# Kernel tuning notes

Hardware: AMD Instinct MI355X
Metric: run time of the kernel (lower is better)

The kernel has to match this reference:

```python
import jax, jax.numpy as jnp
import numpy as np

B, S, H, NL, DF, VF = 8, 2048, 8, 128, 64, 64
NF, HS = 1280, 33
FEAT = NF + HS
NLAYERS = 2
MAXLAP = 0.001


def setup_inputs() -> dict:
    key = jax.random.key(0)
    ks = jax.random.split(key, 11)
    u = lambda k, shape: jax.random.uniform(k, shape, jnp.float32, -0.01, 0.01)
    return {
        "latent_outputs": jax.random.normal(ks[0], (B, S, HS), jnp.float32),
        "masks": (jax.random.uniform(ks[1], (B, S, 1)) > 0.05).astype(jnp.float32),
        "x_embeds": jax.random.normal(ks[2], (B, S, NF), jnp.float32),
        "pos_embed": jax.random.normal(ks[3], (B, S, DF), jnp.float32),
        "collect_classes": u(ks[4], (1, VF * H, HS)),
        "query_linear": u(ks[5], (NLAYERS, 1, H, FEAT + 1, DF)),
        "key_linear": u(ks[6], (NLAYERS, 1, 1, FEAT + 1, DF)),
        "value_linear": u(ks[7], (NLAYERS, 1, H, FEAT + 1, VF)),
        "project_original": u(ks[8], (NLAYERS, 1, 1, FEAT + 1, VF)),
        "aggregation_params": u(ks[9], (NLAYERS, 1, H, 1, 1)),
        "collect_feats": u(ks[10], (NLAYERS - 1, VF * H, FEAT)),
    }


def _iterative_inv(mat, n_iter=6):
    I = jnp.eye(mat.shape[-1], dtype=mat.dtype)
    key = mat
    value = (1.0 / jnp.max(jnp.sum(key, axis=-2))) * jnp.swapaxes(key, -1, -2)
    for _ in range(n_iter):
        kv = key @ value
        value = 0.25 * value @ (13 * I - kv @ (15 * I - kv @ (7 * I - kv)))
    return value


def _compute_accum(values, masks, qw, kw, vw, agg):
    # values: [B,1,S,FEAT]; qw/vw: [1,H,FEAT+1,*], kw: [1,1,FEAT+1,DF]
    # NOTE: bias is the second-to-last row (as in the torch source, [..., -2:-1, :]).
    Eq = values @ qw[..., :-1, :] + qw[..., -2:-1, :]  # [B,H,S,DF]
    Ek = values @ kw[..., :-1, :] + kw[..., -2:-1, :]  # [B,1,S,DF]
    Ev = values @ vw[..., :-1, :] + vw[..., -2:-1, :]  # [B,H,S,VF]
    pos = jnp.arange(S)
    rel = jnp.abs(pos[None, None, None, :] - pos[None, None, :, None]).astype(values.dtype)
    sigmas = jnp.abs(agg) + MAXLAP          # [1,H,1,1]
    pos_mask = -sigmas * rel                # [1,H,S,S] Laplace position penalty
    scale = DF ** 0.25
    Eq = Eq / scale
    Ek = Ek / scale
    seg = S // NL
    q_land = Eq.reshape(Eq.shape[0], Eq.shape[1], NL, seg, DF).mean(-2)  # [B,H,NL,DF]
    k_land = Ek.reshape(Ek.shape[0], Ek.shape[1], NL, seg, DF).mean(-2)  # [B,1,NL,DF]
    pos_sel = pos_mask.reshape(1, H, NL, seg, S).mean(3)                 # [1,H,NL,S]
    kernel_1 = jax.nn.softmax(Eq @ jnp.swapaxes(k_land, -1, -2)
                              + jnp.swapaxes(pos_sel, -1, -2), axis=-1)  # [B,H,S,NL]
    pos_sel2 = pos_sel.reshape(1, H, NL, NL, seg).mean(-1)               # [1,H,NL,NL]
    kernel_2 = jax.nn.softmax(q_land @ jnp.swapaxes(k_land, -1, -2) + pos_sel2, axis=-1)
    scores = q_land @ jnp.swapaxes(Ek, -1, -2)                            # [B,H,NL,S]
    attn_mask = jnp.swapaxes(jnp.where(masks[:, None] == 0, -1e6, 0.0), -1, -2)  # [B,1,1,S]
    kernel_3 = jax.nn.softmax(scores + attn_mask + pos_sel, axis=-1)      # [B,H,NL,S]
    probs = kernel_1 @ _iterative_inv(kernel_2)                           # [B,H,S,NL]
    return probs @ (kernel_3 @ Ev)                                        # [B,H,S,VF]


def reference(latent_outputs, masks, x_embeds, pos_embed, collect_classes,
              query_linear, key_linear, value_linear, project_original,
              aggregation_params, collect_feats):
    cl = jax.nn.softmax(latent_outputs, axis=-1) * masks
    orig = jnp.concatenate([x_embeds, cl], axis=-1)[:, None]  # [B,1,S,FEAT]
    va = orig
    for layer in range(NLAYERS):
        va = _compute_accum(va, masks, query_linear[layer], key_linear[layer],
                            value_linear[layer], aggregation_params[layer])
        pw = project_original[layer, ..., :-1, :]
        pb = project_original[layer, ..., -2:-1, :]
        va = va + (orig @ pw + pb) / NLAYERS            # [B,H,S,VF]
        va = jnp.transpose(va, (0, 2, 1, 3)).reshape(B, S, H * VF)
        cw = collect_feats[layer] if layer < NLAYERS - 1 else collect_classes
        va = (va @ cw)[:, None]
    return va[:, 0] * masks  # [B,S,HS]
```

## Files before the change

kernel.cpp:

```cpp
#include <hip/hip_runtime.h>
#include <math.h>


namespace {

constexpr int B = 8, S = 2048, H = 8, NL = 128, DF = 64, VF = 64;
constexpr int NF = 1280, HS = 33, FEAT = 1313, FEATP = 1314;
constexpr int SEG = 16, HV = H * VF;
constexpr int KSF = 1344;
constexpr int NSPL = 4;
constexpr long ROWS = (long)B * S;
constexpr float INV_SCALE = 0.35355339059327373f;

typedef _Float16 f16;
typedef _Float16 f16x8 __attribute__((ext_vector_type(8)));
typedef _Float16 f16x4 __attribute__((ext_vector_type(4)));
typedef float f32x4 __attribute__((ext_vector_type(4)));

__global__ __launch_bounds__(256) void k_cl(
    const float* __restrict__ lat, const float* __restrict__ masks,
    float* __restrict__ cl)
{
  long row = (long)blockIdx.x * 4 + (threadIdx.x >> 6);
  int l = threadIdx.x & 63;
  float v = (l < HS) ? lat[row * HS + l] : -INFINITY;
  float m = v;
  #pragma unroll
  for (int o = 32; o; o >>= 1) m = fmaxf(m, __shfl_xor(m, o));
  float e = (l < HS) ? expf(v - m) : 0.f;
  float s = e;
  #pragma unroll
  for (int o = 32; o; o >>= 1) s += __shfl_xor(s, o);
  if (l < HS) cl[row * HS + l] = e / s * masks[row];
}

__global__ __launch_bounds__(256) void k_prep(
    const float* __restrict__ xemb, const float* __restrict__ cl,
    const float* __restrict__ qlin, const float* __restrict__ klin,
    const float* __restrict__ vlin, const float* __restrict__ plin,
    const float* __restrict__ cfeat, const float* __restrict__ ccls,
    f16* __restrict__ origA,
    f16* __restrict__ WQt, f16* __restrict__ WKt, f16* __restrict__ WVt,
    f16* __restrict__ WPt, f16* __restrict__ WCFt, f16* __restrict__ WCCt)
{
  long bid = blockIdx.x;
  int tid = threadIdx.x;
  if (bid < 10752) {
    long idx = bid * 256 + tid;
    long row = idx / 168;
    int c = (int)(idx - row * 168);
    int t = c >> 3, cs = c & 7;
    int k0 = t * 64 + cs * 8;
    f16x8 v;
    if (t < 20) {
      float4 a = *(const float4*)&xemb[row * NF + k0];
      float4 b = *(const float4*)&xemb[row * NF + k0 + 4];
      v[0] = (f16)a.x; v[1] = (f16)a.y; v[2] = (f16)a.z; v[3] = (f16)a.w;
      v[4] = (f16)b.x; v[5] = (f16)b.y; v[6] = (f16)b.z; v[7] = (f16)b.w;
    } else {
      #pragma unroll
      for (int i = 0; i < 8; ++i) {
        int k = k0 + i;
        float f = 0.f;
        if (k < NF) f = xemb[row * NF + k];
        else if (k < FEAT) f = cl[row * HS + (k - NF)];
        v[i] = (f16)f;
      }
    }
    int cd = cs ^ ((int)row & 7);
    *(f16x8*)&origA[row * KSF + t * 64 + cd * 8] = v;
  } else {
    constexpr long s1 = 172032, s2 = 193536, s3 = 365568, s4 = 387072,
                   s5 = 473088, s6 = 477184;
    long idx = (bid - 10752) * 256 + tid;
    if (idx >= s6) return;
    const float* src; f16* dst; int K, N, Npad, KS; long srcZ, rel;
    if (idx < s1)      { src = qlin;  dst = WQt;  K = FEAT; N = 64;  Npad = 64;  KS = KSF; srcZ = (long)FEATP * 64; rel = idx; }
    else if (idx < s2) { src = klin;  dst = WKt;  K = FEAT; N = 64;  Npad = 64;  KS = KSF; srcZ = (long)FEATP * 64; rel = idx - s1; }
    else if (idx < s3) { src = vlin;  dst = WVt;  K = FEAT; N = 64;  Npad = 64;  KS = KSF; srcZ = (long)FEATP * 64; rel = idx - s2; }
    else if (idx < s4) { src = plin;  dst = WPt;  K = FEAT; N = 64;  Npad = 64;  KS = KSF; srcZ = (long)FEATP * 64; rel = idx - s3; }
    else if (idx < s5) { src = cfeat; dst = WCFt; K = 512;  N = FEAT; Npad = KSF; KS = 512; srcZ = 0; rel = idx - s4; }
    else               { src = ccls;  dst = WCCt; K = 512;  N = HS;  Npad = 64;  KS = 512; srcZ = 0; rel = idx - s5; }
    long cpz = (long)Npad * (KS >> 3);
    long z = rel / cpz;
    long rem = rel - z * cpz;
    int n = (int)(rem / (KS >> 3));
    int c = (int)(rem - (long)n * (KS >> 3));
    int t = c >> 3, cs = c & 7;
    int cd = cs ^ (n & 7);
    int k0 = t * 64 + cd * 8;
    const float* sp = src + z * srcZ;
    f16x8 v;
    #pragma unroll
    for (int i = 0; i < 8; ++i) {
      int k = k0 + i;
      v[i] = (f16)((k < K && n < N) ? sp[(long)k * N + n] : 0.f);
    }
    *(f16x8*)&dst[rel * 8] = v;
  }
}

__global__ __launch_bounds__(256, 2) void k_mgemm(
    const f16* __restrict__ A, long aZOff, int aDiv,
    const f16* __restrict__ Wt, long wZOff, int wMod,
    int KT, int mode,
    float* __restrict__ C, long cZOff, int ldC,
    const float* __restrict__ biasBase, long biasZOff, float scale,
    f16* __restrict__ outA, int NR, const float* __restrict__ mask)
{
  const long KS = (long)KT * 64;
  int z = blockIdx.z;
  const f16* Ap = A + (long)(z / aDiv) * aZOff;
  const f16* Wp = Wt + (long)(z % wMod) * wZOff;
  long m0 = (long)blockIdx.x * 256;
  int n0 = blockIdx.y * 64;
  constexpr int BOFF = 256 * 64;
  __shared__ f16 lds[2][(256 + 64) * 64];
  int tid = threadIdx.x;
  int wv = tid >> 6, l = tid & 63;

  const f16* aW = Ap + (m0 + wv * 64 + (l >> 3)) * KS + (l & 7) * 8;
  const f16* bW = Wp + ((long)(n0 + wv * 16 + (l >> 3))) * KS + (l & 7) * 8;

  f32x4 acc[4][4];
  #pragma unroll
  for (int i = 0; i < 4; ++i)
    #pragma unroll
    for (int j = 0; j < 4; ++j) acc[i][j] = (f32x4){0.f, 0.f, 0.f, 0.f};

  auto stage = [&](int buf, int t) {
    f16* la = &lds[buf][(wv * 64) * 64];
    const f16* ga = aW + (long)t * 64;
    #pragma unroll
    for (int j = 0; j < 8; ++j)
      __builtin_amdgcn_global_load_lds(
          (const __attribute__((address_space(1))) void*)(ga + (long)j * 8 * KS),
          (__attribute__((address_space(3))) void*)(la + j * 8 * 64), 16, 0, 0);
    f16* lb = &lds[buf][BOFF + (wv * 16) * 64];
    const f16* gb = bW + (long)t * 64;
    #pragma unroll
    for (int j = 0; j < 2; ++j)
      __builtin_amdgcn_global_load_lds(
          (const __attribute__((address_space(1))) void*)(gb + (long)j * 8 * KS),
          (__attribute__((address_space(3))) void*)(lb + j * 8 * 64), 16, 0, 0);
  };

  stage(0, 0);
  int rA = (wv * 64 + (l & 15)) * 64;
  int rB = BOFF + (l & 15) * 64;
  int lc = l >> 4, lx = l & 7;
  for (int t = 0; t < KT; ++t) {
    int nb = t & 1;
    if (t + 1 < KT) {
      stage(nb ^ 1, t + 1);
      asm volatile("s_waitcnt vmcnt(10)" ::: "memory");
    } else {
      asm volatile("s_waitcnt vmcnt(0)" ::: "memory");
    }
    __syncthreads();
    const f16* base = &lds[nb][0];
    f16x8 af[4][2], bf[4][2];
    #pragma unroll
    for (int mi = 0; mi < 4; ++mi)
      #pragma unroll
      for (int kh = 0; kh < 2; ++kh)
        af[mi][kh] = *(const f16x8*)&base[rA + mi * 16 * 64 + (((kh * 4 + lc) ^ lx) << 3)];
    #pragma unroll
    for (int ni = 0; ni < 4; ++ni)
      #pragma unroll
      for (int kh = 0; kh < 2; ++kh)
        bf[ni][kh] = *(const f16x8*)&base[rB + ni * 16 * 64 + (((kh * 4 + lc) ^ lx) << 3)];
    #pragma unroll
    for (int mi = 0; mi < 4; ++mi)
      #pragma unroll
      for (int ni = 0; ni < 4; ++ni) {
        acc[mi][ni] = __builtin_amdgcn_mfma_f32_16x16x32_f16(af[mi][0], bf[ni][0], acc[mi][ni], 0, 0, 0);
        acc[mi][ni] = __builtin_amdgcn_mfma_f32_16x16x32_f16(af[mi][1], bf[ni][1], acc[mi][ni], 0, 0, 0);
      }
    __syncthreads();
  }

  int lr = (l >> 4) * 4;
  int lcn = l & 15;
  if (mode == 2) {
    #pragma unroll
    for (int mi = 0; mi < 4; ++mi) {
      #pragma unroll
      for (int r = 0; r < 4; ++r) {
        long row = m0 + wv * 64 + mi * 16 + lr + r;
        float mv = mask[row];
        #pragma unroll
        for (int ni = 0; ni < 4; ++ni) {
          int col = n0 + ni * 16 + lcn;
          if (col < NR) C[row * (long)ldC + col] = acc[mi][ni][r] * mv;
        }
      }
    }
  } else {
    f16* st = &lds[0][0];
    #pragma unroll
    for (int ni = 0; ni < 4; ++ni) {
      int coll = ni * 16 + lcn;
      int col = n0 + coll;
      bool ok = col < NR;
      #pragma unroll
      for (int mi = 0; mi < 4; ++mi) {
        int rowl = wv * 64 + mi * 16 + lr;
        #pragma unroll
        for (int r = 0; r < 4; ++r) {
          float v = ok ? acc[mi][ni][r] * scale : 0.f;
          st[(rowl + r) * 64 + coll] = (f16)v;
        }
      }
    }
    __syncthreads();
    int tt = n0 >> 6;
    for (int c = tid; c < 2048; c += 256) {
      int row = c >> 3, cd = c & 7;
      long grow = m0 + row;
      int r7 = (int)grow & 7;
      f16x8 v = *(const f16x8*)&st[row * 64 + cd * 8];
      *(f16x8*)&outA[grow * KSF + tt * 64 + ((cd ^ r7) << 3)] = v;
    }
  }
}

__global__ __launch_bounds__(256, 2) void k_qve(
    const f16* __restrict__ Aact, const f16* __restrict__ Aorig,
    const f16* __restrict__ WQl, const f16* __restrict__ WVl,
    const f16* __restrict__ wk, const f16* __restrict__ wp,
    const float* __restrict__ bqBase, const float* __restrict__ bvBase,
    const float* __restrict__ bk, const float* __restrict__ bp,
    f16* __restrict__ Eq16, f16* __restrict__ Ev16, f16* __restrict__ Ek16,
    float* __restrict__ projb,
    f16* __restrict__ qland16, f16* __restrict__ kland16)
{
  constexpr int KT = 21;
  __shared__ __align__(16) f16 shbuf[256 * 64];
  int bid = blockIdx.x;
  int tid = threadIdx.x;
  int wv = tid >> 6, l = tid & 63;
  int l15 = l & 15, lc = l >> 4, lx = l & 7;
  int lr = (l >> 4) * 4;
  int lcn = l & 15;

  if (bid < 1024) {
    constexpr int BOFF = 128 * 64;
    int z = bid >> 4;
    int h = z & 7;
    const f16* Ap = Aact + (long)(z >> 3) * S * KSF;
    const f16* wqp = WQl + (long)h * 64 * KSF;
    const f16* wvp = WVl + (long)h * 64 * KSF;
    const float* bq = bqBase + (long)h * FEATP * 64;
    const float* bv = bvBase + (long)h * FEATP * 64;
    long m0 = (long)(bid & 15) * 128;

    const f16* aW = Ap + (m0 + wv * 32 + (l >> 3)) * KSF + (l & 7) * 8;

    f32x4 acc[2][8];
    #pragma unroll
    for (int i = 0; i < 2; ++i)
      #pragma unroll
      for (int j = 0; j < 8; ++j) acc[i][j] = (f32x4){0.f, 0.f, 0.f, 0.f};

    auto stage = [&](int t) {
      f16* la = &shbuf[(wv * 32) * 64];
      const f16* ga = aW + (long)t * 64;
      #pragma unroll
      for (int j = 0; j < 4; ++j)
        __builtin_amdgcn_global_load_lds(
            (const __attribute__((address_space(1))) void*)(ga + (long)j * 8 * KSF),
            (__attribute__((address_space(3))) void*)(la + j * 512), 16, 0, 0);
      f16* lb = &shbuf[BOFF + (wv * 32) * 64];
      #pragma unroll
      for (int j = 0; j < 4; ++j) {
        int brow = wv * 32 + j * 8 + (l >> 3);
        const f16* src = (brow < 64 ? wqp + (long)brow * KSF
                                    : wvp + (long)(brow - 64) * KSF)
                         + (l & 7) * 8 + (long)t * 64;
        __builtin_amdgcn_global_load_lds(
            (const __attribute__((address_space(1))) void*)src,
            (__attribute__((address_space(3))) void*)(lb + j * 512), 16, 0, 0);
      }
    };

    for (int t = 0; t < KT; ++t) {
      stage(t);
      asm volatile("s_waitcnt vmcnt(0)" ::: "memory");
      __syncthreads();
      const f16* base = &shbuf[0];
      f16x8 af[2][2], bf[8][2];
      #pragma unroll
      for (int mi = 0; mi < 2; ++mi)
        #pragma unroll
        for (int kh = 0; kh < 2; ++kh)
          af[mi][kh] = *(const f16x8*)&base[(wv * 32 + mi * 16 + l15) * 64 + (((kh * 4 + lc) ^ lx) << 3)];
      #pragma unroll
      for (int ni = 0; ni < 8; ++ni) {
        int n = ni * 16 + l15;
        #pragma unroll
        for (int kh = 0; kh < 2; ++kh)
          bf[ni][kh] = *(const f16x8*)&base[BOFF + n * 64 + (((kh * 4 + lc) ^ (n & 7)) << 3)];
      }
      #pragma unroll
      for (int mi = 0; mi < 2; ++mi)
        #pragma unroll
        for (int ni = 0; ni < 8; ++ni) {
          acc[mi][ni] = __builtin_amdgcn_mfma_f32_16x16x32_f16(af[mi][0], bf[ni][0], acc[mi][ni], 0, 0, 0);
          acc[mi][ni] = __builtin_amdgcn_mfma_f32_16x16x32_f16(af[mi][1], bf[ni][1], acc[mi][ni], 0, 0, 0);
        }
      __syncthreads();
    }

    f16* st = &shbuf[0];
    #pragma unroll
    for (int ni = 0; ni < 8; ++ni) {
      int col = ni * 16 + l15;
      float bvv = (col < 64) ? bq[col] : bv[col - 64];
      float scl = (col < 64) ? INV_SCALE : 1.f;
      #pragma unroll
      for (int mi = 0; mi < 2; ++mi) {
        int rowl = wv * 32 + mi * 16 + lr;
        #pragma unroll
        for (int r = 0; r < 4; ++r)
          st[(rowl + r) * 128 + col] = (f16)((acc[mi][ni][r] + bvv) * scl);
      }
    }
    __syncthreads();
    f16* oq = Eq16 + (long)z * S * 64;
    f16* ov = Ev16 + (long)z * S * 64;
    for (int c = tid; c < 1024; c += 256) {
      int rw = c >> 3, cc = c & 7;
      *(f16x8*)&oq[(m0 + rw) * 64 + cc * 8] = *(const f16x8*)&st[rw * 128 + cc * 8];
      *(f16x8*)&ov[(m0 + rw) * 64 + cc * 8] = *(const f16x8*)&st[rw * 128 + 64 + cc * 8];
    }
    for (int c = tid; c < 512; c += 256) {
      int lm = c >> 6, d = c & 63;
      float s = 0.f;
      #pragma unroll
      for (int i = 0; i < SEG; ++i) s += (float)st[(lm * SEG + i) * 128 + d];
      float v = s * (1.f / SEG);
      long li = (long)z * NL + (m0 >> 4) + lm;
      qland16[li * 64 + d] = (f16)v;
    }
  } else {
    constexpr int BOFF = 128 * 64;
    int rel = bid - 1024;
    int zz2 = rel >> 4;
    int prob = zz2 >> 3, b = zz2 & 7;
    const f16* Ap = (prob ? Aorig : Aact) + (long)b * S * KSF;
    const f16* Wp = prob ? wp : wk;
    long m0 = (long)(rel & 15) * 128;

    const f16* aW = Ap + (m0 + wv * 32 + (l >> 3)) * KSF + (l & 7) * 8;
    const f16* bW = Wp + ((long)(wv * 16 + (l >> 3))) * KSF + (l & 7) * 8;

    f32x4 acc[2][4];
    #pragma unroll
    for (int i = 0; i < 2; ++i)
      #pragma unroll
      for (int j = 0; j < 4; ++j) acc[i][j] = (f32x4){0.f, 0.f, 0.f, 0.f};

    auto stage = [&](int t) {
      f16* la = &shbuf[(wv * 32) * 64];
      const f16* ga = aW + (long)t * 64;
      #pragma unroll
      for (int j = 0; j < 4; ++j)
        __builtin_amdgcn_global_load_lds(
            (const __attribute__((address_space(1))) void*)(ga + (long)j * 8 * KSF),
            (__attribute__((address_space(3))) void*)(la + j * 512), 16, 0, 0);
      f16* lb = &shbuf[BOFF + (wv * 16) * 64];
      const f16* gb = bW + (long)t * 64;
      #pragma unroll
      for (int j = 0; j < 2; ++j)
        __builtin_amdgcn_global_load_lds(
            (const __attribute__((address_space(1))) void*)(gb + (long)j * 8 * KSF),
            (__attribute__((address_space(3))) void*)(lb + j * 512), 16, 0, 0);
    };

    for (int t = 0; t < KT; ++t) {
      stage(t);
      asm volatile("s_waitcnt vmcnt(0)" ::: "memory");
      __syncthreads();
      const f16* base = &shbuf[0];
      f16x8 af[2][2], bf[4][2];
      #pragma unroll
      for (int mi = 0; mi < 2; ++mi)
        #pragma unroll
        for (int kh = 0; kh < 2; ++kh)
          af[mi][kh] = *(const f16x8*)&base[(wv * 32 + mi * 16 + l15) * 64 + (((kh * 4 + lc) ^ lx) << 3)];
      #pragma unroll
      for (int ni = 0; ni < 4; ++ni)
        #pragma unroll
        for (int kh = 0; kh < 2; ++kh)
          bf[ni][kh] = *(const f16x8*)&base[BOFF + (ni * 16 + l15) * 64 + (((kh * 4 + lc) ^ lx) << 3)];
      #pragma unroll
      for (int mi = 0; mi < 2; ++mi)
        #pragma unroll
        for (int ni = 0; ni < 4; ++ni) {
          acc[mi][ni] = __builtin_amdgcn_mfma_f32_16x16x32_f16(af[mi][0], bf[ni][0], acc[mi][ni], 0, 0, 0);
          acc[mi][ni] = __builtin_amdgcn_mfma_f32_16x16x32_f16(af[mi][1], bf[ni][1], acc[mi][ni], 0, 0, 0);
        }
      __syncthreads();
    }

    if (prob == 0) {
      f16* st = &shbuf[0];
      #pragma unroll
      for (int ni = 0; ni < 4; ++ni) {
        int col = ni * 16 + lcn;
        float bv = bk[col];
        #pragma unroll
        for (int mi = 0; mi < 2; ++mi) {
          int rowl = wv * 32 + mi * 16 + lr;
          #pragma unroll
          for (int r = 0; r < 4; ++r)
            st[(rowl + r) * 64 + col] = (f16)((acc[mi][ni][r] + bv) * INV_SCALE);
        }
      }
      __syncthreads();
      f16* o16 = Ek16 + (long)b * S * 64;
      for (int c = tid; c < 1024; c += 256) {
        int row = c >> 3, cc = c & 7;
        f16x8 v = *(const f16x8*)&st[row * 64 + cc * 8];
        *(f16x8*)&o16[(m0 + row) * 64 + cc * 8] = v;
      }
      for (int c = tid; c < 512; c += 256) {
        int lm = c >> 6, d = c & 63;
        float s = 0.f;
        #pragma unroll
        for (int i = 0; i < SEG; ++i) s += (float)st[(lm * SEG + i) * 64 + d];
        float v = s * (1.f / SEG);
        long li = (long)b * NL + (m0 >> 4) + lm;
        kland16[li * 64 + d] = (f16)v;
      }
    } else {
      float* Cp = projb + (long)b * S * 64;
      #pragma unroll
      for (int ni = 0; ni < 4; ++ni) {
        int col = ni * 16 + lcn;
        float bv = bp[col];
        #pragma unroll
        for (int mi = 0; mi < 2; ++mi) {
          long row = m0 + wv * 32 + mi * 16 + lr;
          #pragma unroll
          for (int r = 0; r < 4; ++r)
            Cp[(row + r) * 64 + col] = (acc[mi][ni][r] + bv) * 0.5f;
        }
      }
    }
  }
}

__global__ __launch_bounds__(256, 2) void k_land(
    const f16* __restrict__ qland16, const f16* __restrict__ kland16,
    const f16* __restrict__ Ek16, const f16* __restrict__ Ev16,
    const float* __restrict__ aggL, const float* __restrict__ masks,
    float* __restrict__ partU, float* __restrict__ partML,
    f16* __restrict__ k2h, float* __restrict__ colmax)
{
  __shared__ __align__(16) unsigned char smem[57856];
  int bid = blockIdx.x;
  int tid = threadIdx.x;
  int w = tid >> 6, l = tid & 63;
  int l15 = l & 15, lg4 = l >> 4, l7 = l & 7;

  if (bid < 512) {
    f16* Qs = (f16*)smem;
    f16* Ks = (f16*)(smem + 8192);
    f16* Vt = (f16*)(smem + 24576);
    f16* Pb = (f16*)(smem + 40960);
    float* Ms = (float*)(smem + 57344);
    int chunk = bid & (NSPL - 1);
    int z2 = bid >> 2;
    int z = z2 >> 1, half = z2 & 1;
    int b = z >> 3, h = z & 7;
    int q0 = half * 64;
    float sigma = fabsf(aggL[h]) + 0.001f;
    float cpos = -sigma * (1.f / 16.f);

    for (int c = tid; c < 64 * 8; c += 256) {
      int q = c >> 3, kc = c & 7;
      f16x8 v = *(const f16x8*)&qland16[((long)z * NL + q0 + q) * 64 + kc * 8];
      *(f16x8*)&Qs[q * 64 + ((kc ^ (q & 7)) << 3)] = v;
    }

    f16* Pw = &Pb[w * 16 * 128];
    f32x4 Oa[4];
    #pragma unroll
    for (int i = 0; i < 4; ++i) Oa[i] = (f32x4){0.f, 0.f, 0.f, 0.f};
    float mrun[4] = {-INFINITY, -INFINITY, -INFINITY, -INFINITY};
    float lrun[4] = {0.f, 0.f, 0.f, 0.f};

    int t0beg = chunk * (S / 128 / NSPL), t0end = t0beg + S / 128 / NSPL;
    for (int t0 = t0beg; t0 < t0end; ++t0) {
      __syncthreads();
      for (int c = tid; c < 1024; c += 256) {
        int k = c >> 3, kc = c & 7;
        f16x8 v = *(const f16x8*)&Ek16[((long)b * S + t0 * 128 + k) * 64 + kc * 8];
        *(f16x8*)&Ks[k * 64 + ((kc ^ (k & 7)) << 3)] = v;
      }
      for (int c = tid; c < 1024; c += 256) {
        int k = c & 127, dc = c >> 7;
        f16x8 v = *(const f16x8*)&Ev16[((long)z * S + t0 * 128 + k) * 64 + dc * 8];
        int kc = k >> 3, ki = k & 7;
        #pragma unroll
        for (int j = 0; j < 8; ++j) {
          int d = dc * 8 + j;
          Vt[d * 128 + ((kc ^ (d & 7)) << 3) + ki] = v[j];
        }
      }
      if (tid < 128)
        Ms[tid] = (masks[(long)b * S + t0 * 128 + tid] == 0.f) ? -1e6f : 0.f;
      __syncthreads();

      f16x8 af[2];
      #pragma unroll
      for (int kh = 0; kh < 2; ++kh)
        af[kh] = *(const f16x8*)&Qs[(w * 16 + l15) * 64 + (((kh * 4 + lg4) ^ l7) << 3)];
      f32x4 sc[8];
      #pragma unroll
      for (int ct = 0; ct < 8; ++ct) {
        int n = ct * 16 + l15;
        f16x8 b0 = *(const f16x8*)&Ks[n * 64 + (((lg4) ^ (n & 7)) << 3)];
        f16x8 b1 = *(const f16x8*)&Ks[n * 64 + (((4 + lg4) ^ (n & 7)) << 3)];
        f32x4 zz = (f32x4){0.f, 0.f, 0.f, 0.f};
        zz = __builtin_amdgcn_mfma_f32_16x16x32_f16(af[0], b0, zz, 0, 0, 0);
        sc[ct] = __builtin_amdgcn_mfma_f32_16x16x32_f16(af[1], b1, zz, 0, 0, 0);
      }
      float tmax[4] = {-INFINITY, -INFINITY, -INFINITY, -INFINITY};
      #pragma unroll
      for (int ct = 0; ct < 8; ++ct) {
        float mk = Ms[ct * 16 + l15];
        int key = t0 * 128 + ct * 16 + l15;
        #pragma unroll
        for (int r = 0; r < 4; ++r) {
          int qg = q0 + w * 16 + lg4 * 4 + r;
          float a = (float)(key - 16 * qg);
          float ac = fminf(fmaxf(a, 0.f), 15.f);
          float dd = fabsf(a - ac);
          float sum = ac * ac - 15.f * ac + 120.f + 16.f * dd;
          float s = sc[ct][r] + cpos * sum + mk;
          sc[ct][r] = s;
          tmax[r] = fmaxf(tmax[r], s);
        }
      }
      #pragma unroll
      for (int r = 0; r < 4; ++r) {
        #pragma unroll
        for (int o = 1; o < 16; o <<= 1)
          tmax[r] = fmaxf(tmax[r], __shfl_xor(tmax[r], o));
      }
      float fr[4], lsum[4];
      #pragma unroll
      for (int r = 0; r < 4; ++r) {
        float mnew = fmaxf(mrun[r], tmax[r]);
        fr[r] = expf(mrun[r] - mnew);
        mrun[r] = mnew;
        lsum[r] = 0.f;
      }
      #pragma unroll
      for (int ct = 0; ct < 8; ++ct) {
        #pragma unroll
        for (int r = 0; r < 4; ++r) {
          float p = expf(sc[ct][r] - mrun[r]);
          sc[ct][r] = p;
          lsum[r] += p;
        }
      }
      #pragma unroll
      for (int r = 0; r < 4; ++r) {
        #pragma unroll
        for (int o = 1; o < 16; o <<= 1)
          lsum[r] += __shfl_xor(lsum[r], o);
        lrun[r] = lrun[r] * fr[r] + lsum[r];
      }
      f32x4 fv = (f32x4){fr[0], fr[1], fr[2], fr[3]};
      #pragma unroll
      for (int dt = 0; dt < 4; ++dt) Oa[dt] *= fv;
      #pragma unroll
      for (int ct = 0; ct < 8; ++ct) {
        int kc = ct * 2 + (l15 >> 3);
        int ki = l15 & 7;
        #pragma unroll
        for (int r = 0; r < 4; ++r) {
          int row = lg4 * 4 + r;
          Pw[row * 128 + ((kc ^ (row & 7)) << 3) + ki] = (f16)sc[ct][r];
        }
      }
      #pragma unroll
      for (int ks = 0; ks < 4; ++ks) {
        f16x8 pa = *(const f16x8*)&Pw[l15 * 128 + (((ks * 4 + lg4) ^ l7) << 3)];
        #pragma unroll
        for (int dt = 0; dt < 4; ++dt) {
          int n = dt * 16 + l15;
          f16x8 bv = *(const f16x8*)&Vt[n * 128 + (((ks * 4 + lg4) ^ (n & 7)) << 3)];
          Oa[dt] = __builtin_amdgcn_mfma_f32_16x16x32_f16(pa, bv, Oa[dt], 0, 0, 0);
        }
      }
    }
    #pragma unroll
    for (int r = 0; r < 4; ++r) {
      long qg = q0 + w * 16 + lg4 * 4 + r;
      long base = ((long)z * NL + qg) * NSPL + chunk;
      #pragma unroll
      for (int dt = 0; dt < 4; ++dt)
        partU[base * 64 + dt * 16 + l15] = Oa[dt][r];
      if (l15 == 0) {
        partML[base * 2] = mrun[r];
        partML[base * 2 + 1] = lrun[r];
      }
    }
  } else {
    f16* Qs2 = (f16*)smem;
    f16* Ks2 = (f16*)(smem + 16384);
    float* colpart = (float*)(smem + 32768);
    int z = bid - 512;
    int b2 = z >> 3, h2 = z & 7;
    float sigma = fabsf(aggL[h2]) + 0.001f;
    for (int c = tid; c < 1024; c += 256) {
      int q = c >> 3, kc = c & 7;
      f16x8 v = *(const f16x8*)&qland16[((long)z * NL + q) * 64 + kc * 8];
      *(f16x8*)&Qs2[q * 64 + ((kc ^ (q & 7)) << 3)] = v;
      f16x8 u = *(const f16x8*)&kland16[((long)b2 * NL + q) * 64 + kc * 8];
      *(f16x8*)&Ks2[q * 64 + ((kc ^ (q & 7)) << 3)] = u;
    }
    __syncthreads();
    f32x4 acc[2][8];
    #pragma unroll
    for (int i = 0; i < 2; ++i)
      #pragma unroll
      for (int j = 0; j < 8; ++j) acc[i][j] = (f32x4){0.f, 0.f, 0.f, 0.f};
    f16x8 af[2][2];
    #pragma unroll
    for (int mi = 0; mi < 2; ++mi)
      #pragma unroll
      for (int kh = 0; kh < 2; ++kh)
        af[mi][kh] = *(const f16x8*)&Qs2[(w * 32 + mi * 16 + l15) * 64 + (((kh * 4 + lg4) ^ l7) << 3)];
    #pragma unroll
    for (int ni = 0; ni < 8; ++ni) {
      int n = ni * 16 + l15;
      f16x8 b0 = *(const f16x8*)&Ks2[n * 64 + ((lg4 ^ (n & 7)) << 3)];
      f16x8 b1 = *(const f16x8*)&Ks2[n * 64 + (((4 + lg4) ^ (n & 7)) << 3)];
      #pragma unroll
      for (int mi = 0; mi < 2; ++mi) {
        acc[mi][ni] = __builtin_amdgcn_mfma_f32_16x16x32_f16(af[mi][0], b0, acc[mi][ni], 0, 0, 0);
        acc[mi][ni] = __builtin_amdgcn_mfma_f32_16x16x32_f16(af[mi][1], b1, acc[mi][ni], 0, 0, 0);
      }
    }
    float colp[8];
    #pragma unroll
    for (int ni = 0; ni < 8; ++ni) colp[ni] = 0.f;
    f16* o2 = k2h + (long)z * NL * NL;
    #pragma unroll
    for (int mi = 0; mi < 2; ++mi) {
      float tmax[4] = {-INFINITY, -INFINITY, -INFINITY, -INFINITY};
      #pragma unroll
      for (int ni = 0; ni < 8; ++ni) {
        int m = ni * 16 + l15;
        #pragma unroll
        for (int r = 0; r < 4; ++r) {
          int row = w * 32 + mi * 16 + lg4 * 4 + r;
          float dd = fabsf((float)(row - m));
          float s = acc[mi][ni][r] - sigma * ((row == m) ? 5.3125f : 16.f * dd);
          acc[mi][ni][r] = s;
          tmax[r] = fmaxf(tmax[r], s);
        }
      }
      #pragma unroll
      for (int r = 0; r < 4; ++r) {
        #pragma unroll
        for (int o = 1; o < 16; o <<= 1)
          tmax[r] = fmaxf(tmax[r], __shfl_xor(tmax[r], o));
      }
      float lsum2[4] = {0.f, 0.f, 0.f, 0.f};
      #pragma unroll
      for (int ni = 0; ni < 8; ++ni)
        #pragma unroll
        for (int r = 0; r < 4; ++r) {
          float e = expf(acc[mi][ni][r] - tmax[r]);
          acc[mi][ni][r] = e;
          lsum2[r] += e;
        }
      #pragma unroll
      for (int r = 0; r < 4; ++r) {
        #pragma unroll
        for (int o = 1; o < 16; o <<= 1)
          lsum2[r] += __shfl_xor(lsum2[r], o);
        lsum2[r] = 1.f / lsum2[r];
      }
      #pragma unroll
      for (int ni = 0; ni < 8; ++ni) {
        int m = ni * 16 + l15;
        #pragma unroll
        for (int r = 0; r < 4; ++r) {
          float p = acc[mi][ni][r] * lsum2[r];
          o2[(long)(w * 32 + mi * 16 + lg4 * 4 + r) * NL + m] = (f16)p;
          colp[ni] += p;
        }
      }
    }
    #pragma unroll
    for (int ni = 0; ni < 8; ++ni) {
      colp[ni] += __shfl_xor(colp[ni], 16);
      colp[ni] += __shfl_xor(colp[ni], 32);
    }
    if (lg4 == 0) {
      #pragma unroll
      for (int ni = 0; ni < 8; ++ni)
        colpart[w * 128 + ni * 16 + l15] = colp[ni];
    }
    __syncthreads();
    if (tid < 128) {
      float cs = colpart[tid] + colpart[128 + tid] + colpart[256 + tid] + colpart[384 + tid];
      float wm = cs;
      #pragma unroll
      for (int o = 32; o; o >>= 1) wm = fmaxf(wm, __shfl_xor(wm, o));
      if ((tid & 63) == 0) colpart[512 + (tid >> 6)] = wm;
    }
    __syncthreads();
    if (tid == 0) colmax[z] = fmaxf(colpart[512], colpart[513]);
  }
}

__global__ __launch_bounds__(512) void k_inverse(
    const f16* __restrict__ k2h, const float* __restrict__ colmax,
    const float* __restrict__ partU, const float* __restrict__ partML,
    float* __restrict__ m2)
{
  __shared__ __align__(16) f16 bufA[128 * 128];
  __shared__ __align__(16) f16 bufB[128 * 128];
  __shared__ __align__(16) f16 Vt[128 * 128];
  __shared__ __align__(16) f16 Pt[128 * 128];
  int z = blockIdx.x;
  int tid = threadIdx.x;
  int w = tid >> 6, l = tid & 63;
  int l15 = l & 15, lg4 = l >> 4;
  int wr = (w >> 1) * 32, wc = (w & 1) * 64;

  float cv = colmax[l];
  #pragma unroll
  for (int o = 32; o; o >>= 1) cv = fmaxf(cv, __shfl_xor(cv, o));
  float recip = 1.f / cv;

  const f16* key = k2h + (long)z * NL * NL;
  auto swz = [](int r, int c) { return r * 128 + ((((c >> 3) ^ (r & 15))) << 3) + (c & 7); };

  for (int idx = tid; idx < 128 * 16; idx += 512) {
    int r = idx >> 4, c8 = (idx & 15) << 3;
    f16x8 kk = *(const f16x8*)&key[r * 128 + c8];
    f16x8 sv;
    #pragma unroll
    for (int j = 0; j < 8; ++j) sv[j] = (f16)(recip * (float)kk[j]);
    *(f16x8*)&Vt[swz(r, c8)] = sv;
    #pragma unroll
    for (int j = 0; j < 8; ++j) bufA[swz(c8 + j, r)] = sv[j];
  }
  __syncthreads();

  f16* Vc = bufA;
  f16* Sc = bufB;

  f32x4 acc[2][4];
  auto MMc = [&](bool fromGlobal, const f16* Aimg, const f16* Bimg) {
    #pragma unroll
    for (int mi = 0; mi < 2; ++mi)
      #pragma unroll
      for (int ni = 0; ni < 4; ++ni) acc[mi][ni] = (f32x4){0.f, 0.f, 0.f, 0.f};
    #pragma unroll
    for (int ks = 0; ks < 4; ++ks) {
      int k0 = ks * 32 + lg4 * 8;
      f16x8 bf[4];
      #pragma unroll
      for (int ni = 0; ni < 4; ++ni)
        bf[ni] = *(const f16x8*)&Bimg[swz(wc + ni * 16 + l15, k0)];
      f16x8 af[2];
      if (fromGlobal) {
        af[0] = *(const f16x8*)&key[(wr + l15) * 128 + k0];
        af[1] = *(const f16x8*)&key[(wr + 16 + l15) * 128 + k0];
      } else {
        af[0] = *(const f16x8*)&Aimg[swz(wr + l15, k0)];
        af[1] = *(const f16x8*)&Aimg[swz(wr + 16 + l15, k0)];
      }
      #pragma unroll
      for (int mi = 0; mi < 2; ++mi)
        #pragma unroll
        for (int ni = 0; ni < 4; ++ni)
          acc[mi][ni] = __builtin_amdgcn_mfma_f32_16x16x32_f16(af[mi], bf[ni], acc[mi][ni], 0, 0, 0);
    }
  };
  auto store = [&](f16* Nout, f16* Tout, float aT, float bT) {
    #pragma unroll
    for (int mi = 0; mi < 2; ++mi) {
      int row0 = wr + mi * 16 + lg4 * 4;
      #pragma unroll
      for (int ni = 0; ni < 4; ++ni) {
        int col = wc + ni * 16 + l15;
        f16x4 tv;
        #pragma unroll
        for (int r = 0; r < 4; ++r) {
          float v = acc[mi][ni][r];
          if (Nout) Nout[swz(row0 + r, col)] = (f16)v;
          tv[r] = (f16)(aT * v + ((row0 + r == col) ? bT : 0.f));
        }
        *(f16x4*)&Tout[col * 128 + ((((row0 >> 3) ^ (col & 15))) << 3) + (row0 & 7)] = tv;
      }
    }
  };

  for (int it = 0; it < 6; ++it) {
    MMc(true, nullptr, Vt);  store(Sc, Pt, -1.f, 7.f);       __syncthreads();
    MMc(false, Sc, Pt);      store(nullptr, Vt, -1.f, 15.f); __syncthreads();
    MMc(false, Sc, Vt);      store(nullptr, Pt, -0.25f, 3.25f); __syncthreads();
    MMc(false, Vc, Pt);      store(Sc, Vt, 1.f, 0.f);        __syncthreads();
    f16* tsw = Vc; Vc = Sc; Sc = tsw;
  }

  for (int idx = tid; idx < 128 * 16; idx += 512) {
    int q = idx >> 4, c4 = (idx & 15) << 2;
    long base = ((long)z * NL + q) * NSPL;
    float m[NSPL], lv[NSPL];
    #pragma unroll
    for (int c = 0; c < NSPL; ++c) {
      m[c] = partML[(base + c) * 2];
      lv[c] = partML[(base + c) * 2 + 1];
    }
    float M = fmaxf(fmaxf(m[0], m[1]), fmaxf(m[2], m[3]));
    float L = 0.f, scf[NSPL];
    #pragma unroll
    for (int c = 0; c < NSPL; ++c) {
      scf[c] = expf(m[c] - M);
      L += lv[c] * scf[c];
    }
    float4 o = make_float4(0.f, 0.f, 0.f, 0.f);
    #pragma unroll
    for (int c = 0; c < NSPL; ++c) {
      float4 u = *(const float4*)&partU[(base + c) * 64 + c4];
      o.x += scf[c] * u.x; o.y += scf[c] * u.y;
      o.z += scf[c] * u.z; o.w += scf[c] * u.w;
    }
    float invL = 1.f / L;
    Pt[swz(c4 + 0, q)] = (f16)(o.x * invL);
    Pt[swz(c4 + 1, q)] = (f16)(o.y * invL);
    Pt[swz(c4 + 2, q)] = (f16)(o.z * invL);
    Pt[swz(c4 + 3, q)] = (f16)(o.w * invL);
  }
  __syncthreads();
  f32x4 accF[4];
  #pragma unroll
  for (int ni = 0; ni < 4; ++ni) accF[ni] = (f32x4){0.f, 0.f, 0.f, 0.f};
  #pragma unroll
  for (int ks = 0; ks < 4; ++ks) {
    int k0 = ks * 32 + lg4 * 8;
    f16x8 af = *(const f16x8*)&Vc[swz(w * 16 + l15, k0)];
    #pragma unroll
    for (int ni = 0; ni < 4; ++ni) {
      f16x8 bf = *(const f16x8*)&Pt[swz(ni * 16 + l15, k0)];
      accF[ni] = __builtin_amdgcn_mfma_f32_16x16x32_f16(af, bf, accF[ni], 0, 0, 0);
    }
  }
  float* mp = m2 + (long)z * NL * VF;
  #pragma unroll
  for (int ni = 0; ni < 4; ++ni)
    #pragma unroll
    for (int r = 0; r < 4; ++r)
      mp[(long)(w * 16 + lg4 * 4 + r) * VF + ni * 16 + l15] = accF[ni][r];
}

__global__ __launch_bounds__(256, 2) void k_k1attn(
    const f16* __restrict__ Eq16, const f16* __restrict__ kland16,
    const float* __restrict__ aggL, const float* __restrict__ m2,
    const float* __restrict__ proj, f16* __restrict__ merged)
{
  __shared__ __align__(16) f16 Kl[128 * 64];
  __shared__ __align__(16) f16 M2t[64 * 128];
  __shared__ __align__(16) f16 Pb[4 * 16 * 128];
  int zz = blockIdx.x;
  int z = zz >> 5, st = zz & 31;
  int b = z >> 3, h = z & 7;
  int s0 = st * 64;
  int tid = threadIdx.x;
  int w = tid >> 6, l = tid & 63;
  int l15 = l & 15, lg4 = l >> 4, l7 = l & 7;
  float sigma = fabsf(aggL[h]) + 0.001f;
  float cpos = -sigma * (1.f / 16.f);

  for (int c = tid; c < 128 * 8; c += 256) {
    int k = c >> 3, kc = c & 7;
    f16x8 v = *(const f16x8*)&kland16[((long)b * NL + k) * 64 + kc * 8];
    *(f16x8*)&Kl[k * 64 + ((kc ^ (k & 7)) << 3)] = v;
  }
  const float* mp = m2 + (long)z * NL * VF;
  for (int c = tid; c < 128 * 16; c += 256) {
    int k = c >> 4, c4 = (c & 15) << 2;
    float4 v4 = *(const float4*)&mp[k * 64 + c4];
    int kc = k >> 3, ki = k & 7;
    M2t[(c4 + 0) * 128 + ((kc ^ ((c4 + 0) & 7)) << 3) + ki] = (f16)v4.x;
    M2t[(c4 + 1) * 128 + ((kc ^ ((c4 + 1) & 7)) << 3) + ki] = (f16)v4.y;
    M2t[(c4 + 2) * 128 + ((kc ^ ((c4 + 2) & 7)) << 3) + ki] = (f16)v4.z;
    M2t[(c4 + 3) * 128 + ((kc ^ ((c4 + 3) & 7)) << 3) + ki] = (f16)v4.w;
  }
  __syncthreads();

  long qrow = (long)z * S + s0 + w * 16 + l15;
  f16x8 af[2];
  #pragma unroll
  for (int kh = 0; kh < 2; ++kh)
    af[kh] = *(const f16x8*)&Eq16[qrow * 64 + kh * 32 + lg4 * 8];

  f32x4 sc[8];
  #pragma unroll
  for (int ct = 0; ct < 8; ++ct) {
    int n = ct * 16 + l15;
    f16x8 b0 = *(const f16x8*)&Kl[n * 64 + ((lg4 ^ (n & 7)) << 3)];
    f16x8 b1 = *(const f16x8*)&Kl[n * 64 + (((4 + lg4) ^ (n & 7)) << 3)];
    f32x4 zz4 = (f32x4){0.f, 0.f, 0.f, 0.f};
    zz4 = __builtin_amdgcn_mfma_f32_16x16x32_f16(af[0], b0, zz4, 0, 0, 0);
    sc[ct] = __builtin_amdgcn_mfma_f32_16x16x32_f16(af[1], b1, zz4, 0, 0, 0);
  }
  float tmax[4] = {-INFINITY, -INFINITY, -INFINITY, -INFINITY};
  #pragma unroll
  for (int ct = 0; ct < 8; ++ct) {
    int lm = ct * 16 + l15;
    #pragma unroll
    for (int r = 0; r < 4; ++r) {
      int spos = s0 + w * 16 + lg4 * 4 + r;
      float a = (float)(spos - 16 * lm);
      float ac = fminf(fmaxf(a, 0.f), 15.f);
      float dd = fabsf(a - ac);
      float sum = ac * ac - 15.f * ac + 120.f + 16.f * dd;
      float s = sc[ct][r] + cpos * sum;
      sc[ct][r] = s;
      tmax[r] = fmaxf(tmax[r], s);
    }
  }
  #pragma unroll
  for (int r = 0; r < 4; ++r) {
    #pragma unroll
    for (int o = 1; o < 16; o <<= 1)
      tmax[r] = fmaxf(tmax[r], __shfl_xor(tmax[r], o));
  }
  float lsum[4] = {0.f, 0.f, 0.f, 0.f};
  #pragma unroll
  for (int ct = 0; ct < 8; ++ct) {
    #pragma unroll
    for (int r = 0; r < 4; ++r) {
      float p = expf(sc[ct][r] - tmax[r]);
      sc[ct][r] = p;
      lsum[r] += p;
    }
  }
  #pragma unroll
  for (int r = 0; r < 4; ++r) {
    #pragma unroll
    for (int o = 1; o < 16; o <<= 1)
      lsum[r] += __shfl_xor(lsum[r], o);
    lsum[r] = 1.f / lsum[r];
  }
  f16* Pw = &Pb[w * 16 * 128];
  #pragma unroll
  for (int ct = 0; ct < 8; ++ct) {
    int kc = ct * 2 + (l15 >> 3);
    int ki = l15 & 7;
    #pragma unroll
    for (int r = 0; r < 4; ++r) {
      int row = lg4 * 4 + r;
      Pw[row * 128 + ((kc ^ (row & 7)) << 3) + ki] = (f16)(sc[ct][r] * lsum[r]);
    }
  }
  f32x4 Oa[4];
  #pragma unroll
  for (int i = 0; i < 4; ++i) Oa[i] = (f32x4){0.f, 0.f, 0.f, 0.f};
  #pragma unroll
  for (int ks = 0; ks < 4; ++ks) {
    f16x8 pa = *(const f16x8*)&Pw[l15 * 128 + (((ks * 4 + lg4) ^ l7) << 3)];
    #pragma unroll
    for (int dt = 0; dt < 4; ++dt) {
      int n = dt * 16 + l15;
      f16x8 bv = *(const f16x8*)&M2t[n * 128 + (((ks * 4 + lg4) ^ (n & 7)) << 3)];
      Oa[dt] = __builtin_amdgcn_mfma_f32_16x16x32_f16(pa, bv, Oa[dt], 0, 0, 0);
    }
  }
  #pragma unroll
  for (int r = 0; r < 4; ++r) {
    long srow = (long)b * S + s0 + w * 16 + lg4 * 4 + r;
    int r7 = (int)(srow & 7);
    #pragma unroll
    for (int dt = 0; dt < 4; ++dt) {
      int col = dt * 16 + l15;
      float v = Oa[dt][r] + proj[srow * VF + col];
      merged[srow * (long)HV + h * 64 + (((col >> 3) ^ r7) << 3) + (col & 7)] = (f16)v;
    }
  }
}

}

extern "C" void kernel_launch(void* const* d_in, const int* in_sizes, int n_in,
                              void* d_out, int out_size, void* d_ws, size_t ws_size,
                              hipStream_t stream)
{
  const float* lat   = (const float*)d_in[0];
  const float* masks = (const float*)d_in[1];
  const float* xemb  = (const float*)d_in[2];
  const float* ccls  = (const float*)d_in[4];
  const float* qlin  = (const float*)d_in[5];
  const float* klin  = (const float*)d_in[6];
  const float* vlin  = (const float*)d_in[7];
  const float* plin  = (const float*)d_in[8];
  const float* agg   = (const float*)d_in[9];
  const float* cfeat = (const float*)d_in[10];
  float* out = (float*)d_out;
  float* ws = (float*)d_ws;

  long off = 0;
  auto allocF = [&](long n) { float* p = ws + off; off += (n + 3) & ~3L; return p; };
  auto allocH = [&](long n) { f16* p = (f16*)(ws + off); off += ((n + 1) / 2 + 3) & ~3L; return p; };

  f16* origA = allocH(ROWS * KSF);
  f16* vbufA = allocH(ROWS * KSF);
  f16* merged = allocH(ROWS * (long)HV);
  f16* WQt = allocH(16L * 64 * KSF);
  f16* WKt = allocH(2L * 64 * KSF);
  f16* WVt = allocH(16L * 64 * KSF);
  f16* WPt = allocH(2L * 64 * KSF);
  f16* WCFt = allocH((long)KSF * 512);
  f16* WCCt = allocH(64L * 512);
  f16* Ek16 = allocH((long)B * S * 64);
  f16* Ev16 = allocH((long)B * H * S * 64);
  f16* Eq16 = allocH((long)B * H * S * 64);
  f16* qland16 = allocH((long)B * H * NL * DF);
  f16* kland16 = allocH((long)B * NL * DF);
  f16* k2h = allocH((long)B * H * NL * NL);
  float* cl     = allocF(ROWS * HS);
  float* projb  = allocF((long)B * S * VF);
  float* m2b    = allocF((long)B * H * NL * VF);
  float* colmax = allocF(64);
  float* partU  = allocF((long)B * H * NL * NSPL * 64);
  float* partML = allocF((long)B * H * NL * NSPL * 2);

  k_cl<<<(int)(ROWS / 4), 256, 0, stream>>>(lat, masks, cl);
  k_prep<<<10752 + 1864, 256, 0, stream>>>(xemb, cl, qlin, klin, vlin, plin,
      cfeat, ccls, origA, WQt, WKt, WVt, WPt, WCFt, WCCt);

  const f16* Aact = origA;
  for (int layer = 0; layer < 2; ++layer) {
    const f16* wq = WQt + (long)layer * 8 * 64 * KSF;
    const f16* wk = WKt + (long)layer * 64 * KSF;
    const f16* wvv = WVt + (long)layer * 8 * 64 * KSF;
    const f16* wp = WPt + (long)layer * 64 * KSF;
    const float* bq = qlin + (long)layer * 8 * FEATP * 64 + (long)(FEATP - 2) * 64;
    const float* bk = klin + (long)layer * FEATP * 64 + (long)(FEATP - 2) * 64;
    const float* bv = vlin + (long)layer * 8 * FEATP * 64 + (long)(FEATP - 2) * 64;
    const float* bp = plin + (long)layer * FEATP * 64 + (long)(FEATP - 2) * 64;
    const float* ag = agg + layer * H;

    k_qve<<<1280, 256, 0, stream>>>(Aact, origA, wq, wvv, wk, wp,
        bq, bv, bk, bp, Eq16, Ev16, Ek16, projb, qland16, kland16);

    k_land<<<576, 256, 0, stream>>>(qland16, kland16, Ek16, Ev16, ag, masks,
        partU, partML, k2h, colmax);
    k_inverse<<<B * H, 512, 0, stream>>>(k2h, colmax, partU, partML, m2b);
    k_k1attn<<<B * H * (S / 64), 256, 0, stream>>>(Eq16, kland16, ag, m2b, projb, merged);

    if (layer == 0) {
      dim3 gC(64, 21, 1);
      k_mgemm<<<gC, 256, 0, stream>>>(merged, 0, 1, WCFt, 0, 1, 8, 1,
          nullptr, 0, 0, nullptr, 0, 1.0f, vbufA, FEAT, nullptr);
      Aact = vbufA;
    } else {
      dim3 gO(64, 1, 1);
      k_mgemm<<<gO, 256, 0, stream>>>(merged, 0, 1, WCCt, 0, 1, 8, 2,
          out, 0, HS, nullptr, 0, 1.0f, nullptr, HS, masks);
    }
  }
  (void)in_sizes; (void)n_in; (void)out_size; (void)ws_size;
}
```

Before: 433.7 us.

## Process all 128 landmark queries per block and split keys eight ways

Each landmark-attention block now handles both 64-query halves against the same staged K/V tile, so K and V are loaded into shared memory once for all 128 queries instead of twice. To keep the block count at 512, the key dimension is split into 8 chunks instead of 4, and the merge step now reduces over 8 partials. The cost is more per-thread register state (two sets of accumulators), larger shared memory per block, and more partial results to combine.

```diff
diff --git a/kernel.cpp b/kernel.cpp
--- a/kernel.cpp
+++ b/kernel.cpp
@@ -8,7 +8,7 @@
 constexpr int NF = 1280, HS = 33, FEAT = 1313, FEATP = 1314;
 constexpr int SEG = 16, HV = H * VF;
 constexpr int KSF = 1344;
-constexpr int NSPL = 4;
+constexpr int NSPL = 8;
 constexpr long ROWS = (long)B * S;
 constexpr float INV_SCALE = 0.35355339059327373f;
 
@@ -459,7 +459,7 @@
     float* __restrict__ partU, float* __restrict__ partML,
     f16* __restrict__ k2h, float* __restrict__ colmax)
 {
-  __shared__ __align__(16) unsigned char smem[57856];
+  __shared__ __align__(16) unsigned char smem[66048];
   int bid = blockIdx.x;
   int tid = threadIdx.x;
   int w = tid >> 6, l = tid & 63;
@@ -467,30 +467,33 @@
 
   if (bid < 512) {
     f16* Qs = (f16*)smem;
-    f16* Ks = (f16*)(smem + 8192);
-    f16* Vt = (f16*)(smem + 24576);
-    f16* Pb = (f16*)(smem + 40960);
-    float* Ms = (float*)(smem + 57344);
+    f16* Ks = (f16*)(smem + 16384);
+    f16* Vt = (f16*)(smem + 32768);
+    f16* Pb = (f16*)(smem + 49152);
+    float* Ms = (float*)(smem + 65536);
     int chunk = bid & (NSPL - 1);
-    int z2 = bid >> 2;
-    int z = z2 >> 1, half = z2 & 1;
+    int z = bid >> 3;
     int b = z >> 3, h = z & 7;
-    int q0 = half * 64;
     float sigma = fabsf(aggL[h]) + 0.001f;
     float cpos = -sigma * (1.f / 16.f);
 
-    for (int c = tid; c < 64 * 8; c += 256) {
+    for (int c = tid; c < 128 * 8; c += 256) {
       int q = c >> 3, kc = c & 7;
-      f16x8 v = *(const f16x8*)&qland16[((long)z * NL + q0 + q) * 64 + kc * 8];
+      f16x8 v = *(const f16x8*)&qland16[((long)z * NL + q) * 64 + kc * 8];
       *(f16x8*)&Qs[q * 64 + ((kc ^ (q & 7)) << 3)] = v;
     }
 
     f16* Pw = &Pb[w * 16 * 128];
-    f32x4 Oa[4];
-    #pragma unroll
-    for (int i = 0; i < 4; ++i) Oa[i] = (f32x4){0.f, 0.f, 0.f, 0.f};
-    float mrun[4] = {-INFINITY, -INFINITY, -INFINITY, -INFINITY};
-    float lrun[4] = {0.f, 0.f, 0.f, 0.f};
+    f32x4 Oa[2][4];
+    float mrun[2][4], lrun[2][4];
+    #pragma unroll
+    for (int hf = 0; hf < 2; ++hf)
+      #pragma unroll
+      for (int i = 0; i < 4; ++i) {
+        Oa[hf][i] = (f32x4){0.f, 0.f, 0.f, 0.f};
+        mrun[hf][i] = -INFINITY;
+        lrun[hf][i] = 0.f;
+      }
 
     int t0beg = chunk * (S / 128 / NSPL), t0end = t0beg + S / 128 / NSPL;
     for (int t0 = t0beg; t0 < t0end; ++t0) {
@@ -514,101 +517,108 @@
         Ms[tid] = (masks[(long)b * S + t0 * 128 + tid] == 0.f) ? -1e6f : 0.f;
       __syncthreads();
 
-      f16x8 af[2];
-      #pragma unroll
-      for (int kh = 0; kh < 2; ++kh)
-        af[kh] = *(const f16x8*)&Qs[(w * 16 + l15) * 64 + (((kh * 4 + lg4) ^ l7) << 3)];
-      f32x4 sc[8];
-      #pragma unroll
-      for (int ct = 0; ct < 8; ++ct) {
-        int n = ct * 16 + l15;
-        f16x8 b0 = *(const f16x8*)&Ks[n * 64 + (((lg4) ^ (n & 7)) << 3)];
-        f16x8 b1 = *(const f16x8*)&Ks[n * 64 + (((4 + lg4) ^ (n & 7)) << 3)];
-        f32x4 zz = (f32x4){0.f, 0.f, 0.f, 0.f};
-        zz = __builtin_amdgcn_mfma_f32_16x16x32_f16(af[0], b0, zz, 0, 0, 0);
-        sc[ct] = __builtin_amdgcn_mfma_f32_16x16x32_f16(af[1], b1, zz, 0, 0, 0);
-      }
-      float tmax[4] = {-INFINITY, -INFINITY, -INFINITY, -INFINITY};
-      #pragma unroll
-      for (int ct = 0; ct < 8; ++ct) {
-        float mk = Ms[ct * 16 + l15];
-        int key = t0 * 128 + ct * 16 + l15;
+      #pragma unroll
+      for (int hf = 0; hf < 2; ++hf) {
+        int q0 = hf * 64;
+        f16x8 af[2];
+        #pragma unroll
+        for (int kh = 0; kh < 2; ++kh)
+          af[kh] = *(const f16x8*)&Qs[(q0 + w * 16 + l15) * 64 + (((kh * 4 + lg4) ^ l7) << 3)];
+        f32x4 sc[8];
+        #pragma unroll
+        for (int ct = 0; ct < 8; ++ct) {
+          int n = ct * 16 + l15;
+          f16x8 b0 = *(const f16x8*)&Ks[n * 64 + (((lg4) ^ (n & 7)) << 3)];
+          f16x8 b1 = *(const f16x8*)&Ks[n * 64 + (((4 + lg4) ^ (n & 7)) << 3)];
+          f32x4 zz = (f32x4){0.f, 0.f, 0.f, 0.f};
+          zz = __builtin_amdgcn_mfma_f32_16x16x32_f16(af[0], b0, zz, 0, 0, 0);
+          sc[ct] = __builtin_amdgcn_mfma_f32_16x16x32_f16(af[1], b1, zz, 0, 0, 0);
+        }
+        float tmax[4] = {-INFINITY, -INFINITY, -INFINITY, -INFINITY};
+        #pragma unroll
+        for (int ct = 0; ct < 8; ++ct) {
+          float mk = Ms[ct * 16 + l15];
+          int key = t0 * 128 + ct * 16 + l15;
+          #pragma unroll
+          for (int r = 0; r < 4; ++r) {
+            int qg = q0 + w * 16 + lg4 * 4 + r;
+            float a = (float)(key - 16 * qg);
+            float ac = fminf(fmaxf(a, 0.f), 15.f);
+            float dd = fabsf(a - ac);
+            float sum = ac * ac - 15.f * ac + 120.f + 16.f * dd;
+            float s = sc[ct][r] + cpos * sum + mk;
+            sc[ct][r] = s;
+            tmax[r] = fmaxf(tmax[r], s);
+          }
+        }
         #pragma unroll
         for (int r = 0; r < 4; ++r) {
-          int qg = q0 + w * 16 + lg4 * 4 + r;
-          float a = (float)(key - 16 * qg);
-          float ac = fminf(fmaxf(a, 0.f), 15.f);
-          float dd = fabsf(a - ac);
-          float sum = ac * ac - 15.f * ac + 120.f + 16.f * dd;
-          float s = sc[ct][r] + cpos * sum + mk;
-          sc[ct][r] = s;
-          tmax[r] = fmaxf(tmax[r], s);
-        }
-      }
+          #pragma unroll
+          for (int o = 1; o < 16; o <<= 1)
+            tmax[r] = fmaxf(tmax[r], __shfl_xor(tmax[r], o));
+        }
+        float fr[4], lsum[4];
+        #pragma unroll
+        for (int r = 0; r < 4; ++r) {
+          float mnew = fmaxf(mrun[hf][r], tmax[r]);
+          fr[r] = expf(mrun[hf][r] - mnew);
+          mrun[hf][r] = mnew;
+          lsum[r] = 0.f;
+        }
+        #pragma unroll
+        for (int ct = 0; ct < 8; ++ct) {
+          #pragma unroll
+          for (int r = 0; r < 4; ++r) {
+            float p = expf(sc[ct][r] - mrun[hf][r]);
+            sc[ct][r] = p;
+            lsum[r] += p;
+          }
+        }
+        #pragma unroll
+        for (int r = 0; r < 4; ++r) {
+          #pragma unroll
+          for (int o = 1; o < 16; o <<= 1)
+            lsum[r] += __shfl_xor(lsum[r], o);
+          lrun[hf][r] = lrun[hf][r] * fr[r] + lsum[r];
+        }
+        f32x4 fv = (f32x4){fr[0], fr[1], fr[2], fr[3]};
+        #pragma unroll
+        for (int dt = 0; dt < 4; ++dt) Oa[hf][dt] *= fv;
+        #pragma unroll
+        for (int ct = 0; ct < 8; ++ct) {
+          int kc = ct * 2 + (l15 >> 3);
+          int ki = l15 & 7;
+          #pragma unroll
+          for (int r = 0; r < 4; ++r) {
+            int row = lg4 * 4 + r;
+            Pw[row * 128 + ((kc ^ (row & 7)) << 3) + ki] = (f16)sc[ct][r];
+          }
+        }
+        #pragma unroll
+        for (int ks = 0; ks < 4; ++ks) {
+          f16x8 pa = *(const f16x8*)&Pw[l15 * 128 + (((ks * 4 + lg4) ^ l7) << 3)];
+          #pragma unroll
+          for (int dt = 0; dt < 4; ++dt) {
+            int n = dt * 16 + l15;
+            f16x8 bv = *(const f16x8*)&Vt[n * 128 + (((ks * 4 + lg4) ^ (n & 7)) << 3)];
+            Oa[hf][dt] = __builtin_amdgcn_mfma_f32_16x16x32_f16(pa, bv, Oa[hf][dt], 0, 0, 0);
+          }
+        }
+      }
+    }
+    #pragma unroll
+    for (int hf = 0; hf < 2; ++hf) {
       #pragma unroll
       for (int r = 0; r < 4; ++r) {
-        #pragma unroll
-        for (int o = 1; o < 16; o <<= 1)
-          tmax[r] = fmaxf(tmax[r], __shfl_xor(tmax[r], o));
-      }
-      float fr[4], lsum[4];
-      #pragma unroll
-      for (int r = 0; r < 4; ++r) {
-        float mnew = fmaxf(mrun[r], tmax[r]);
-        fr[r] = expf(mrun[r] - mnew);
-        mrun[r] = mnew;
-        lsum[r] = 0.f;
-      }
-      #pragma unroll
-      for (int ct = 0; ct < 8; ++ct) {
-        #pragma unroll
-        for (int r = 0; r < 4; ++r) {
-          float p = expf(sc[ct][r] - mrun[r]);
-          sc[ct][r] = p;
-          lsum[r] += p;
-        }
-      }
-      #pragma unroll
-      for (int r = 0; r < 4; ++r) {
-        #pragma unroll
-        for (int o = 1; o < 16; o <<= 1)
-          lsum[r] += __shfl_xor(lsum[r], o);
-        lrun[r] = lrun[r] * fr[r] + lsum[r];
-      }
-      f32x4 fv = (f32x4){fr[0], fr[1], fr[2], fr[3]};
-      #pragma unroll
-      for (int dt = 0; dt < 4; ++dt) Oa[dt] *= fv;
-      #pragma unroll
-      for (int ct = 0; ct < 8; ++ct) {
-        int kc = ct * 2 + (l15 >> 3);
-        int ki = l15 & 7;
-        #pragma unroll
-        for (int r = 0; r < 4; ++r) {
-          int row = lg4 * 4 + r;
-          Pw[row * 128 + ((kc ^ (row & 7)) << 3) + ki] = (f16)sc[ct][r];
-        }
-      }
-      #pragma unroll
-      for (int ks = 0; ks < 4; ++ks) {
-        f16x8 pa = *(const f16x8*)&Pw[l15 * 128 + (((ks * 4 + lg4) ^ l7) << 3)];
-        #pragma unroll
-        for (int dt = 0; dt < 4; ++dt) {
-          int n = dt * 16 + l15;
-          f16x8 bv = *(const f16x8*)&Vt[n * 128 + (((ks * 4 + lg4) ^ (n & 7)) << 3)];
-          Oa[dt] = __builtin_amdgcn_mfma_f32_16x16x32_f16(pa, bv, Oa[dt], 0, 0, 0);
-        }
-      }
-    }
-    #pragma unroll
-    for (int r = 0; r < 4; ++r) {
-      long qg = q0 + w * 16 + lg4 * 4 + r;
-      long base = ((long)z * NL + qg) * NSPL + chunk;
-      #pragma unroll
-      for (int dt = 0; dt < 4; ++dt)
-        partU[base * 64 + dt * 16 + l15] = Oa[dt][r];
-      if (l15 == 0) {
-        partML[base * 2] = mrun[r];
-        partML[base * 2 + 1] = lrun[r];
+        long qg = hf * 64 + w * 16 + lg4 * 4 + r;
+        long base = ((long)z * NL + qg) * NSPL + chunk;
+        #pragma unroll
+        for (int dt = 0; dt < 4; ++dt)
+          partU[base * 64 + dt * 16 + l15] = Oa[hf][dt][r];
+        if (l15 == 0) {
+          partML[base * 2] = mrun[hf][r];
+          partML[base * 2 + 1] = lrun[hf][r];
+        }
       }
     }
   } else {
@@ -825,7 +835,9 @@
       m[c] = partML[(base + c) * 2];
       lv[c] = partML[(base + c) * 2 + 1];
     }
-    float M = fmaxf(fmaxf(m[0], m[1]), fmaxf(m[2], m[3]));
+    float M = m[0];
+    #pragma unroll
+    for (int c = 1; c < NSPL; ++c) M = fmaxf(M, m[c]);
     float L = 0.f, scf[NSPL];
     #pragma unroll
     for (int c = 0; c < NSPL; ++c) {
```

New measurement: 448.8 us. 3.5% more time.
